# Optimization experiments

Measured on AMD Instinct MI355X. Metric: run time of the kernel, lower is better.

Reference implementation:

```python
import jax, jax.numpy as jnp
import numpy as np

N, E, Nd, D, F = 100000, 400000, 4096, 512, 8000
EMB = 300
NUM_LAYERS = 5


def setup_inputs() -> dict:
    key = jax.random.key(0)
    ks = iter(jax.random.split(key, 24))
    x = jax.random.randint(next(ks), (N, 2), 0, 3)
    edge_index = jax.random.randint(next(ks), (2, E), 0, N)
    edge_attr = jax.random.randint(next(ks), (E, 2), 0, 3)
    dangling_idx = jax.random.randint(next(ks), (Nd,), 0, N)
    frag_batch = jnp.sort(jax.random.randint(next(ks), (N,), 0, F))
    dangling_edge_index = jax.random.randint(next(ks), (2, D), 0, Nd)
    drop_edge_attr = jax.random.randint(next(ks), (D, 2), 0, 3)
    p = lambda shape: jax.random.normal(next(ks), shape, jnp.float32) * 0.02
    return dict(
        x=x, edge_index=edge_index, edge_attr=edge_attr,
        dangling_idx=dangling_idx, frag_batch=frag_batch,
        dangling_edge_index=dangling_edge_index, drop_edge_attr=drop_edge_attr,
        atom_emb1=p((120, EMB)), atom_emb2=p((3, EMB)),
        gin_ee1=p((NUM_LAYERS, 6, EMB)), gin_ee2=p((NUM_LAYERS, 3, EMB)),
        W1=p((NUM_LAYERS, EMB, 2 * EMB)), b1=jnp.zeros((NUM_LAYERS, 2 * EMB), jnp.float32),
        W2=p((NUM_LAYERS, 2 * EMB, EMB)), b2=jnp.zeros((NUM_LAYERS, EMB), jnp.float32),
        bn_g=jnp.ones((NUM_LAYERS, EMB), jnp.float32), bn_b=jnp.zeros((NUM_LAYERS, EMB), jnp.float32),
        E1=p((6, 4 * EMB * EMB)), E2=p((3, 4 * EMB * EMB)),
    )


def _gnn(x, edge_index, edge_attr, atom_emb1, atom_emb2,
         gin_ee1, gin_ee2, W1, b1, W2, b2, bn_g, bn_b):
    # node features from two categorical embeddings
    h = atom_emb1[x[:, 0]] + atom_emb2[x[:, 1]]  # [N, EMB]
    src, dst = edge_index[0], edge_index[1]
    for l in range(NUM_LAYERS):
        ee = gin_ee1[l][edge_attr[:, 0]] + gin_ee2[l][edge_attr[:, 1]]  # [E, EMB]
        aggr = jax.ops.segment_sum(h[src] + ee, dst, num_segments=N)
        # self-loops with edge_attr = (4, 0)
        aggr = aggr + h + gin_ee1[l][4] + gin_ee2[l][0]
        h = jax.nn.relu(aggr @ W1[l] + b1[l]) @ W2[l] + b2[l]  # GIN MLP
        # BatchNorm1d (training-mode batch statistics), eps=1e-5
        mean = h.mean(axis=0)
        var = h.var(axis=0)
        h = (h - mean) * jax.lax.rsqrt(var + 1e-5) * bn_g[l] + bn_b[l]
        if l < NUM_LAYERS - 1:
            h = jax.nn.relu(h)
    return h


def reference(x, edge_index, edge_attr, dangling_idx, frag_batch,
              dangling_edge_index, drop_edge_attr,
              atom_emb1, atom_emb2, gin_ee1, gin_ee2,
              W1, b1, W2, b2, bn_g, bn_b, E1, E2):
    h = _gnn(x, edge_index, edge_attr, atom_emb1, atom_emb2,
             gin_ee1, gin_ee2, W1, b1, W2, b2, bn_g, bn_b)  # [N, EMB]
    dangling_out = h[dangling_idx]  # [Nd, EMB]
    # global_mean_pool over fragments
    seg_sum = jax.ops.segment_sum(h, frag_batch, num_segments=F)
    cnt = jax.ops.segment_sum(jnp.ones((N, 1), h.dtype), frag_batch, num_segments=F)
    frag_mean = seg_sum / jnp.maximum(cnt, 1.0)
    frag_out = frag_mean[frag_batch][dangling_idx]  # [Nd, EMB]
    out = jnp.concatenate([dangling_out, frag_out], axis=1) / EMB  # [Nd, 2*EMB]
    out0 = out[dangling_edge_index[0]]  # [D, 2*EMB]
    # per-edge dynamic weight matrices [D, 2*EMB, 2*EMB]
    pm = (E1[drop_edge_attr[:, 0]] + E2[drop_edge_attr[:, 1]]).reshape(D, 2 * EMB, 2 * EMB)
    out0 = jnp.einsum('dk,dkm->dm', out0, pm)
    out1 = out[dangling_edge_index[1]]
    out2 = jnp.roll(out1, 1, axis=0)  # shift_k fixed to 1 for determinism
    logits = jnp.concatenate([jnp.sum(out0 * out1, axis=1),
                              jnp.sum(out0 * out2, axis=1)], axis=0)  # [2*D]
    return logits
```

## Files before the change

### kernel.cpp

```cpp
#include <hip/hip_runtime.h>
#include <hip/hip_bf16.h>
#include <stdint.h>

#define NN 100000
#define EE 400000
#define ND 4096
#define DD 512
#define FF 8000
#define EMB 300
#define HID 600
#define NL 5
#define TCH 50176
#define MPAD 100096

typedef unsigned short u16;
typedef _Float16 f16x8 __attribute__((ext_vector_type(8)));
typedef float f32x4 __attribute__((ext_vector_type(4)));
typedef float f32x2 __attribute__((ext_vector_type(2)));

static __device__ inline u16 f2h(float v) {
    union { _Float16 h; u16 u; } c; c.h = (_Float16)v; return c.u;
}
static __device__ inline float h2f(u16 u) {
    union { u16 u; _Float16 h; } c; c.u = u; return (float)c.h;
}
static __device__ inline uint32_t pk2(float a, float b) {
    return (uint32_t)f2h(a) | ((uint32_t)f2h(b) << 16);
}
static __device__ inline f32x2 up2(uint32_t w) {
    f32x2 r; r.x = h2f((u16)(w & 0xffff)); r.y = h2f((u16)(w >> 16)); return r;
}
static __device__ inline int loff(int row, int cb) {
    return row * 32 + ((cb ^ ((row >> 1) & 3)) * 8);
}

static __global__ void k_init_h(const int* __restrict__ x, const float* __restrict__ ae1,
                                const float* __restrict__ ae2, uint32_t* __restrict__ h) {
    int idx = blockIdx.x * 256 + threadIdx.x;
    if (idx >= NN * 160) return;
    int n = idx / 160, cw = idx - n * 160;
    int c = 2 * cw;
    int x0 = x[2 * n], x1 = x[2 * n + 1];
    float v0 = 0.f, v1 = 0.f;
    if (c < EMB)     v0 = ae1[x0 * EMB + c] + ae2[x1 * EMB + c];
    if (c + 1 < EMB) v1 = ae1[x0 * EMB + c + 1] + ae2[x1 * EMB + c + 1];
    h[idx] = pk2(v0, v1);
}

static __global__ void k_count(const int* __restrict__ ei, const int* __restrict__ ea,
                               int* __restrict__ deg, int* __restrict__ cnt1, int* __restrict__ cnt2) {
    int e = blockIdx.x * 256 + threadIdx.x;
    if (e >= EE) return;
    int dst = ei[EE + e];
    atomicAdd(&deg[dst], 1);
    atomicAdd(&cnt1[dst * 3 + ea[2 * e]], 1);
    atomicAdd(&cnt2[dst * 3 + ea[2 * e + 1]], 1);
}

static __global__ void k_scan1(const int* __restrict__ in, int* __restrict__ incl,
                               int* __restrict__ bsum, int L) {
    __shared__ int s[256];
    int t = threadIdx.x, i = blockIdx.x * 256 + t;
    int v = (i < L) ? in[i] : 0;
    s[t] = v; __syncthreads();
    for (int o = 1; o < 256; o <<= 1) {
        int xv = (t >= o) ? s[t - o] : 0; __syncthreads();
        s[t] += xv; __syncthreads();
    }
    if (i < L) incl[i] = s[t];
    if (t == 255) bsum[blockIdx.x] = s[255];
}

static __global__ void k_scan2(const int* __restrict__ bsum, int* __restrict__ boff, int nb) {
    __shared__ int s[1024];
    int t = threadIdx.x;
    int v = (t < nb) ? bsum[t] : 0;
    s[t] = v; __syncthreads();
    for (int o = 1; o < 1024; o <<= 1) {
        int xv = (t >= o) ? s[t - o] : 0; __syncthreads();
        s[t] += xv; __syncthreads();
    }
    if (t < nb) boff[t] = s[t] - v;
}

static __global__ void k_scan3(const int* __restrict__ in, const int* __restrict__ incl,
                               const int* __restrict__ boff, int* __restrict__ op,
                               int* __restrict__ cursor, int L) {
    int i = blockIdx.x * 256 + threadIdx.x;
    if (i >= L) return;
    int ex = incl[i] - in[i] + boff[i / 256];
    op[i] = ex;
    if (cursor) cursor[i] = ex;
    if (i == L - 1) op[L] = ex + in[i];
}

static __global__ void k_scatter(const int* __restrict__ ei, int* __restrict__ cursor,
                                 int* __restrict__ col) {
    int e = blockIdx.x * 256 + threadIdx.x;
    if (e >= EE) return;
    int dst = ei[EE + e], src = ei[e];
    int p = atomicAdd(&cursor[dst], 1);
    col[p] = src;
}

static __global__ void k_aggr(const u16* __restrict__ h, u16* __restrict__ ag,
                              const int* __restrict__ rowptr, const int* __restrict__ col,
                              const int* __restrict__ cnt1, const int* __restrict__ cnt2,
                              const float* __restrict__ ge1l, const float* __restrict__ ge2l,
                              const float* __restrict__ scv, int relu) {
    __shared__ float se[7 * 320];
    for (int idx = threadIdx.x; idx < 7 * 320; idx += 256) {
        int g = idx / 320, c = idx - g * 320;
        float v = 0.f;
        if (c < EMB) {
            if (g < 3) v = ge1l[g * EMB + c];
            else if (g < 6) v = ge2l[(g - 3) * EMB + c];
            else v = ge1l[4 * EMB + c] + ge2l[c];
        }
        se[idx] = v;
    }
    __syncthreads();
    int wv = threadIdx.x >> 6, lane = threadIdx.x & 63;

    int cw[3];
    f32x2 sc2[3], sh2[3];
#pragma unroll
    for (int j = 0; j < 3; j++) {
        cw[j] = lane + 64 * j;
        if (cw[j] < 160) {
            int c = 2 * cw[j];
            if (scv) {
                sc2[j] = *(const f32x2*)&scv[c];
                sh2[j] = *(const f32x2*)&scv[320 + c];
            } else { sc2[j] = (f32x2){1.f, 1.f}; sh2[j] = (f32x2){0.f, 0.f}; }
        }
    }

    for (int g0 = blockIdx.x * 4; g0 < NN; g0 += gridDim.x * 4) {
        int n = g0 + wv;
        if (n >= NN) continue;
        float c1a = (float)cnt1[n * 3], c1b = (float)cnt1[n * 3 + 1], c1c = (float)cnt1[n * 3 + 2];
        float c2a = (float)cnt2[n * 3], c2b = (float)cnt2[n * 3 + 1], c2c = (float)cnt2[n * 3 + 2];

        f32x2 acc[3];
        const uint32_t* hn = (const uint32_t*)(h + (size_t)n * 320);
#pragma unroll
        for (int j = 0; j < 3; j++) {
            if (cw[j] < 160) {
                int c = 2 * cw[j];
                f32x2 v = up2(hn[cw[j]]) * sc2[j] + sh2[j];
                if (relu) { v.x = fmaxf(v.x, 0.f); v.y = fmaxf(v.y, 0.f); }
                acc[j] = v + *(const f32x2*)&se[6 * 320 + c]
                       + c1a * *(const f32x2*)&se[c]
                       + c1b * *(const f32x2*)&se[320 + c]
                       + c1c * *(const f32x2*)&se[640 + c]
                       + c2a * *(const f32x2*)&se[960 + c]
                       + c2b * *(const f32x2*)&se[1280 + c]
                       + c2c * *(const f32x2*)&se[1600 + c];
            }
        }
        int p = rowptr[n], end = rowptr[n + 1];
        for (; p + 4 <= end; p += 4) {
            const uint32_t* h0 = (const uint32_t*)(h + (size_t)col[p] * 320);
            const uint32_t* h1 = (const uint32_t*)(h + (size_t)col[p + 1] * 320);
            const uint32_t* h2 = (const uint32_t*)(h + (size_t)col[p + 2] * 320);
            const uint32_t* h3 = (const uint32_t*)(h + (size_t)col[p + 3] * 320);
            uint32_t w0[3], w1[3], w2[3], w3[3];
#pragma unroll
            for (int j = 0; j < 3; j++) {
                if (cw[j] < 160) {
                    w0[j] = h0[cw[j]]; w1[j] = h1[cw[j]];
                    w2[j] = h2[cw[j]]; w3[j] = h3[cw[j]];
                }
            }
#pragma unroll
            for (int j = 0; j < 3; j++) {
                if (cw[j] < 160) {
                    f32x2 v0 = up2(w0[j]) * sc2[j] + sh2[j];
                    if (relu) { v0.x = fmaxf(v0.x, 0.f); v0.y = fmaxf(v0.y, 0.f); }
                    acc[j] += v0;
                    f32x2 v1 = up2(w1[j]) * sc2[j] + sh2[j];
                    if (relu) { v1.x = fmaxf(v1.x, 0.f); v1.y = fmaxf(v1.y, 0.f); }
                    acc[j] += v1;
                    f32x2 v2 = up2(w2[j]) * sc2[j] + sh2[j];
                    if (relu) { v2.x = fmaxf(v2.x, 0.f); v2.y = fmaxf(v2.y, 0.f); }
                    acc[j] += v2;
                    f32x2 v3 = up2(w3[j]) * sc2[j] + sh2[j];
                    if (relu) { v3.x = fmaxf(v3.x, 0.f); v3.y = fmaxf(v3.y, 0.f); }
                    acc[j] += v3;
                }
            }
        }
        for (; p + 2 <= end; p += 2) {
            const uint32_t* h0 = (const uint32_t*)(h + (size_t)col[p] * 320);
            const uint32_t* h1 = (const uint32_t*)(h + (size_t)col[p + 1] * 320);
            uint32_t w0[3], w1[3];
#pragma unroll
            for (int j = 0; j < 3; j++)
                if (cw[j] < 160) { w0[j] = h0[cw[j]]; w1[j] = h1[cw[j]]; }
#pragma unroll
            for (int j = 0; j < 3; j++) {
                if (cw[j] < 160) {
                    f32x2 v0 = up2(w0[j]) * sc2[j] + sh2[j];
                    if (relu) { v0.x = fmaxf(v0.x, 0.f); v0.y = fmaxf(v0.y, 0.f); }
                    acc[j] += v0;
                    f32x2 v1 = up2(w1[j]) * sc2[j] + sh2[j];
                    if (relu) { v1.x = fmaxf(v1.x, 0.f); v1.y = fmaxf(v1.y, 0.f); }
                    acc[j] += v1;
                }
            }
        }
        for (; p < end; ++p) {
            const uint32_t* hr = (const uint32_t*)(h + (size_t)col[p] * 320);
#pragma unroll
            for (int j = 0; j < 3; j++) {
                if (cw[j] < 160) {
                    f32x2 v = up2(hr[cw[j]]) * sc2[j] + sh2[j];
                    if (relu) { v.x = fmaxf(v.x, 0.f); v.y = fmaxf(v.y, 0.f); }
                    acc[j] += v;
                }
            }
        }
        uint32_t* ao = (uint32_t*)(ag + (size_t)n * 320);
#pragma unroll
        for (int j = 0; j < 3; j++)
            if (cw[j] < 160) ao[cw[j]] = pk2(acc[j].x, acc[j].y);
    }
}

static __global__ void k_packW1(const float* __restrict__ W1, u16* __restrict__ W1p) {
    int idx = blockIdx.x * 256 + threadIdx.x;
    const int per = 640 * 320;
    if (idx >= NL * per) return;
    int l = idx / per, rem = idx % per;
    int n = rem / 320, k = rem % 320;
    float v = (k < EMB && n < HID) ? W1[(size_t)l * EMB * HID + (size_t)k * HID + n] : 0.f;
    W1p[idx] = f2h(v);
}

static __global__ void k_packW2(const float* __restrict__ W2, u16* __restrict__ W2p) {
    int idx = blockIdx.x * 256 + threadIdx.x;
    const int per = 384 * 640;
    if (idx >= NL * per) return;
    int l = idx / per, rem = idx % per;
    int n = rem / 640, k = rem % 640;
    float v = (k < HID && n < EMB) ? W2[(size_t)l * HID * EMB + (size_t)k * EMB + n] : 0.f;
    W2p[idx] = f2h(v);
}

static __global__ void k_packb(const float* __restrict__ b1, const float* __restrict__ b2,
                               float* __restrict__ b1p, float* __restrict__ b2p) {
    int idx = blockIdx.x * 256 + threadIdx.x;
    if (idx < NL * 640) {
        int l = idx / 640, n = idx % 640;
        b1p[idx] = (n < HID) ? b1[l * HID + n] : 0.f;
    } else if (idx < NL * 640 + NL * 384) {
        int j = idx - NL * 640;
        int l = j / 384, n = j % 384;
        b2p[j] = (n < EMB) ? b2[l * EMB + n] : 0.f;
    }
}

static __global__ void k_precompMt(const float* __restrict__ E1, const float* __restrict__ E2,
                                   u16* __restrict__ Mpt) {
    __shared__ float sT[32][33];
    int p = blockIdx.x, mt = blockIdx.y, kt = blockIdx.z;
    int a = p / 3, b = p % 3;
    const float* e1 = E1 + (size_t)a * 360000;
    const float* e2 = E2 + (size_t)b * 360000;
    int tx = threadIdx.x & 31, ty = threadIdx.x >> 5;
#pragma unroll
    for (int it = 0; it < 4; it++) {
        int k = kt * 32 + ty + it * 8;
        int m = mt * 32 + tx;
        float v = 0.f;
        if (k < HID && m < HID) v = e1[k * HID + m] + e2[k * HID + m];
        sT[ty + it * 8][tx] = v;
    }
    __syncthreads();
#pragma unroll
    for (int it = 0; it < 4; it++) {
        int m = mt * 32 + ty + it * 8;
        int k = kt * 32 + tx;
        Mpt[(size_t)p * 640 * 640 + (size_t)m * 640 + k] = f2h(sT[tx][ty + it * 8]);
    }
}

template <int MODE>
static __global__ __launch_bounds__(256) void k_mfma(
        const u16* __restrict__ A, const u16* __restrict__ B,
        const float* __restrict__ bias, u16* __restrict__ Out, int Mc,
        float* __restrict__ colsum, float* __restrict__ colsq) {
    constexpr int BM    = (MODE == 1) ? 128 : 64;
    constexpr int STR   = (MODE == 1) ? 320 : 640;
    constexpr int STRO  = (MODE == 1) ? 640 : 320;
    constexpr int NSTEP = (MODE == 1) ? 10 : 20;
    constexpr int MF = 4;
    constexpr int NF = (MODE == 1) ? 4 : 2;

    __shared__ __align__(16) u16 sA[BM * 32];
    __shared__ __align__(16) u16 sB[128 * 32];

    int tid = threadIdx.x;
    int lane = tid & 63, wv = tid >> 6;
    int wm = (MODE == 1) ? (wv >> 1) : 0;
    int wn = (MODE == 1) ? (wv & 1) : wv;
    int m0 = blockIdx.y * BM;
    int n0 = blockIdx.x * 128;
    int sr = tid >> 2, scb = tid & 3;

    uint4 rA0, rA1, rB0, rB1;
    auto do_load = [&](int ks) {
        int kk = ks * 32;
        const u16* as = A + (size_t)(m0 + sr) * STR + kk + scb * 8;
        rA0 = *(const uint4*)as;
        if (MODE == 1) rA1 = *(const uint4*)(as + (size_t)64 * STR);
        const u16* bs = B + (size_t)(n0 + sr) * STR + kk + scb * 8;
        rB0 = *(const uint4*)bs;
        rB1 = *(const uint4*)(bs + (size_t)64 * STR);
    };
    do_load(0);

    f32x4 acc[MF][NF];
#pragma unroll
    for (int i = 0; i < MF; i++)
#pragma unroll
        for (int j = 0; j < NF; j++) {
            acc[i][j][0] = 0.f; acc[i][j][1] = 0.f; acc[i][j][2] = 0.f; acc[i][j][3] = 0.f;
        }

    int lrow = lane & 15, lcb = lane >> 4;
    for (int ks = 0; ks < NSTEP; ++ks) {
        __syncthreads();
        *(uint4*)&sA[loff(sr, scb)] = rA0;
        if (MODE == 1) *(uint4*)&sA[loff(sr + 64, scb)] = rA1;
        *(uint4*)&sB[loff(sr, scb)] = rB0;
        *(uint4*)&sB[loff(sr + 64, scb)] = rB1;
        __syncthreads();
        if (ks + 1 < NSTEP) do_load(ks + 1);
        f16x8 af[MF], bfr[NF];
#pragma unroll
        for (int mf = 0; mf < MF; ++mf) {
            int r = wm * 64 + mf * 16 + lrow;
            af[mf] = *(const f16x8*)&sA[loff(r, lcb)];
        }
#pragma unroll
        for (int nf = 0; nf < NF; ++nf) {
            int r = wn * (NF * 16) + nf * 16 + lrow;
            bfr[nf] = *(const f16x8*)&sB[loff(r, lcb)];
        }
#pragma unroll
        for (int mf = 0; mf < MF; ++mf)
#pragma unroll
            for (int nf = 0; nf < NF; ++nf)
                acc[mf][nf] = __builtin_amdgcn_mfma_f32_16x16x32_f16(af[mf], bfr[nf], acc[mf][nf], 0, 0, 0);
    }

    int lrow4 = (lane >> 4) * 4, lcol = lane & 15;
    if (MODE == 1) {
#pragma unroll
        for (int mf = 0; mf < MF; ++mf)
#pragma unroll
            for (int nf = 0; nf < NF; ++nf) {
                int colg = n0 + wn * 64 + nf * 16 + lcol;
                float bv = bias[colg];
#pragma unroll
                for (int rg = 0; rg < 4; ++rg) {
                    int rowl = m0 + wm * 64 + mf * 16 + lrow4 + rg;
                    float v = fmaxf(acc[mf][nf][rg] + bv, 0.f);
                    Out[(size_t)rowl * STRO + colg] = f2h(v);
                }
            }
    } else {
#pragma unroll
        for (int nf = 0; nf < NF; ++nf) {
            int colg = n0 + wn * 32 + nf * 16 + lcol;
            float bv = bias[colg];
            float s = 0.f, q = 0.f;
#pragma unroll
            for (int mf = 0; mf < MF; ++mf)
#pragma unroll
                for (int rg = 0; rg < 4; ++rg) {
                    int rowl = m0 + mf * 16 + lrow4 + rg;
                    float v = acc[mf][nf][rg] + bv;
                    if (rowl < Mc) {
                        s += v; q += v * v;
                        if (colg < EMB) Out[(size_t)rowl * STRO + colg] = f2h(v);
                    }
                }
            s += __shfl_xor(s, 16); s += __shfl_xor(s, 32);
            q += __shfl_xor(q, 16); q += __shfl_xor(q, 32);
            if (lane < 16) { atomicAdd(&colsum[colg], s); atomicAdd(&colsq[colg], q); }
        }
    }
}

static __global__ void k_bnfinal(const float* __restrict__ colsum, const float* __restrict__ colsq,
                                 const float* __restrict__ g, const float* __restrict__ b,
                                 float* __restrict__ scv) {
    int c = threadIdx.x;
    if (c >= 320) return;
    if (c >= EMB) { scv[c] = 0.f; scv[320 + c] = 0.f; return; }
    float mean = colsum[c] * (1.f / NN);
    float var = colsq[c] * (1.f / NN) - mean * mean;
    float rs = rsqrtf(var + 1e-5f);
    float sc = rs * g[c];
    scv[c] = sc;
    scv[320 + c] = b[c] - mean * sc;
}

static __global__ void k_fragcnt(const int* __restrict__ fb, int* __restrict__ fcnt) {
    int i = blockIdx.x * 256 + threadIdx.x;
    if (i >= NN) return;
    atomicAdd(&fcnt[fb[i]], 1);
}

static __global__ void k_fragmean(const u16* __restrict__ h, const int* __restrict__ fstart,
                                  const float* __restrict__ scv, float* __restrict__ fm) {
    int wv = threadIdx.x >> 6, lane = threadIdx.x & 63;
    int f = blockIdx.x * 4 + wv;
    if (f >= FF) return;
    int beg = fstart[f], end = fstart[f + 1];
    float inv = (end > beg) ? 1.f / (float)(end - beg) : 0.f;
    float a0[3], a1[3]; int cw[3];
#pragma unroll
    for (int j = 0; j < 3; j++) { cw[j] = lane + 64 * j; a0[j] = 0.f; a1[j] = 0.f; }
    for (int r = beg; r < end; ++r) {
        const uint32_t* hr = (const uint32_t*)(h + (size_t)r * 320);
#pragma unroll
        for (int j = 0; j < 3; j++)
            if (cw[j] < 160) {
                uint32_t hv = hr[cw[j]];
                a0[j] += h2f((u16)(hv & 0xffff)); a1[j] += h2f((u16)(hv >> 16));
            }
    }
#pragma unroll
    for (int j = 0; j < 3; j++) {
        int c = 2 * cw[j];
        if (c < EMB)
            fm[(size_t)f * EMB + c] = (end > beg) ? (a0[j] * inv * scv[c] + scv[320 + c]) : 0.f;
        if (c + 1 < EMB)
            fm[(size_t)f * EMB + c + 1] = (end > beg) ? (a1[j] * inv * scv[c + 1] + scv[321 + c]) : 0.f;
    }
}

static __global__ void k_build_out(const u16* __restrict__ h, const float* __restrict__ fm,
                                   const int* __restrict__ didx, const int* __restrict__ fb,
                                   const float* __restrict__ scv, u16* __restrict__ outb16) {
    int idx = blockIdx.x * 256 + threadIdx.x;
    if (idx >= ND * 640) return;
    int d = idx / 640, c = idx - d * 640;
    int n = didx[d];
    float v = 0.f;
    if (c < EMB)          v = (h2f(h[(size_t)n * 320 + c]) * scv[c] + scv[320 + c]) * (1.f / EMB);
    else if (c < 2 * EMB) v = fm[(size_t)fb[n] * EMB + (c - EMB)] * (1.f / EMB);
    outb16[idx] = f2h(v);
}

static __global__ void k_bucket(const int* __restrict__ dea, int* __restrict__ eord,
                                int* __restrict__ tm, int* __restrict__ ntl) {
    __shared__ int cnt[9], off[9], cur[9];
    __shared__ short pe[DD];
    int tid = threadIdx.x;
    for (int i = tid; i < 768; i += 256) eord[i] = -1;
    if (tid < 9) { cnt[tid] = 0; cur[tid] = 0; }
    __syncthreads();
    for (int e = tid; e < DD; e += 256) {
        int p = dea[2 * e] * 3 + dea[2 * e + 1];
        pe[e] = (short)p;
        atomicAdd(&cnt[p], 1);
    }
    __syncthreads();
    if (tid == 0) {
        int o = 0, tt = 0;
        for (int p = 0; p < 9; p++) {
            off[p] = o;
            int nt = (cnt[p] + 15) >> 4;
            for (int t = 0; t < nt; t++) { tm[2 * tt] = p; tm[2 * tt + 1] = o + 16 * t; tt++; }
            o += nt * 16;
        }
        *ntl = tt;
    }
    __syncthreads();
    for (int e = tid; e < DD; e += 256) {
        int p = pe[e];
        int slot = off[p] + atomicAdd(&cur[p], 1);
        eord[slot] = e;
    }
}

static __global__ void k_vgather(const u16* __restrict__ outb16, const int* __restrict__ eord,
                                 const int* __restrict__ dei, u16* __restrict__ Vg) {
    int idx = blockIdx.x * 256 + threadIdx.x;
    if (idx >= 768 * 80) return;
    int slot = idx / 80, cb = idx - slot * 80;
    int d = eord[slot];
    uint4 v = {0u, 0u, 0u, 0u};
    if (d >= 0) v = *(const uint4*)&outb16[(size_t)dei[d] * 640 + cb * 8];
    *(uint4*)&Vg[(size_t)slot * 640 + cb * 8] = v;
}

static __global__ __launch_bounds__(256) void k_out0m(
        const u16* __restrict__ Vg, const u16* __restrict__ Mpt,
        const int* __restrict__ tm, const int* __restrict__ ntl,
        const int* __restrict__ eord, float* __restrict__ o0) {
    int bx = blockIdx.x;
    if (bx >= *ntl) return;
    int p = tm[2 * bx], row0 = tm[2 * bx + 1];
    __shared__ __align__(16) u16 sA[16 * 32];
    __shared__ __align__(16) u16 sB[640 * 32];
    int tid = threadIdx.x, lane = tid & 63, wv = tid >> 6;
    const u16* Bb = Mpt + (size_t)p * 640 * 640;
    f32x4 acc[10];
#pragma unroll
    for (int j = 0; j < 10; j++) { acc[j][0]=0.f; acc[j][1]=0.f; acc[j][2]=0.f; acc[j][3]=0.f; }
    int lrow = lane & 15, lcb = lane >> 4;
    for (int ks = 0; ks < 20; ks++) {
        int kk = ks * 32;
        __syncthreads();
        if (tid < 64) {
            int row = tid >> 2, cb = tid & 3;
            *(uint4*)&sA[loff(row, cb)] = *(const uint4*)&Vg[(size_t)(row0 + row) * 640 + kk + cb * 8];
        }
#pragma unroll
        for (int j = 0; j < 10; j++) {
            int i = tid + j * 256, row = i >> 2, cb = i & 3;
            *(uint4*)&sB[loff(row, cb)] = *(const uint4*)&Bb[(size_t)row * 640 + kk + cb * 8];
        }
        __syncthreads();
        f16x8 af = *(const f16x8*)&sA[loff(lrow, lcb)];
#pragma unroll
        for (int nf = 0; nf < 10; nf++) {
            f16x8 bf = *(const f16x8*)&sB[loff(wv * 160 + nf * 16 + lrow, lcb)];
            acc[nf] = __builtin_amdgcn_mfma_f32_16x16x32_f16(af, bf, acc[nf], 0, 0, 0);
        }
    }
    int lrow4 = (lane >> 4) * 4, lcol = lane & 15;
#pragma unroll
    for (int nf = 0; nf < 10; nf++) {
        int col = wv * 160 + nf * 16 + lcol;
#pragma unroll
        for (int rg = 0; rg < 4; rg++) {
            int row = lrow4 + rg;
            int e = eord[row0 + row];
            if (e >= 0 && col < HID) o0[(size_t)e * 640 + col] = acc[nf][rg];
        }
    }
}

static __global__ void k_logits(const float* __restrict__ o0, const u16* __restrict__ outb16,
                                const int* __restrict__ dei, float* __restrict__ dout) {
    int d = blockIdx.x;
    int tid = threadIdx.x, lane = tid & 63;
    int which = tid >> 6;
    int dsel = which ? (d + DD - 1) % DD : d;
    const float* a = o0 + (size_t)d * 640;
    const u16* bv = outb16 + (size_t)dei[DD + dsel] * 640;
    float s = 0.f;
    for (int c = lane; c < HID; c += 64) s += a[c] * h2f(bv[c]);
    for (int o = 32; o > 0; o >>= 1) s += __shfl_down(s, o);
    if (lane == 0) dout[which ? DD + d : d] = s;
}

extern "C" void kernel_launch(void* const* d_in, const int* in_sizes, int n_in,
                              void* d_out, int out_size, void* d_ws, size_t ws_size,
                              hipStream_t stream) {
    const int* x    = (const int*)d_in[0];
    const int* ei   = (const int*)d_in[1];
    const int* ea   = (const int*)d_in[2];
    const int* didx = (const int*)d_in[3];
    const int* fb   = (const int*)d_in[4];
    const int* dei  = (const int*)d_in[5];
    const int* dea  = (const int*)d_in[6];
    const float* ae1 = (const float*)d_in[7];
    const float* ae2 = (const float*)d_in[8];
    const float* ge1 = (const float*)d_in[9];
    const float* ge2 = (const float*)d_in[10];
    const float* W1  = (const float*)d_in[11];
    const float* b1  = (const float*)d_in[12];
    const float* W2  = (const float*)d_in[13];
    const float* b2  = (const float*)d_in[14];
    const float* bng = (const float*)d_in[15];
    const float* bnb = (const float*)d_in[16];
    const float* E1  = (const float*)d_in[17];
    const float* E2  = (const float*)d_in[18];
    float* dout = (float*)d_out;

    char* w = (char*)d_ws;
    auto alloc = [&](size_t bytes) -> void* {
        void* p = (void*)w;
        w += (bytes + 255) & ~(size_t)255;
        return p;
    };
    u16* h   = (u16*)alloc((size_t)MPAD * 320 * 2);
    u16* ag  = (u16*)alloc((size_t)MPAD * 320 * 2);
    u16* t   = (u16*)alloc((size_t)TCH * 640 * 2);
    u16* W1p = (u16*)alloc((size_t)NL * 640 * 320 * 2);
    u16* W2p = (u16*)alloc((size_t)NL * 384 * 640 * 2);
    u16* Mpt = (u16*)alloc((size_t)9 * 640 * 640 * 2);
    float* b1p = (float*)alloc((size_t)NL * 640 * 4);
    float* b2p = (float*)alloc((size_t)NL * 384 * 4);
    int* rowptr = (int*)alloc((size_t)(NN + 1) * 4);
    int* cursor = (int*)alloc((size_t)NN * 4);
    int* col    = (int*)alloc((size_t)EE * 4);
    int* deg    = (int*)alloc((size_t)NN * 4);
    int* cnt1   = (int*)alloc((size_t)NN * 3 * 4);
    int* cnt2   = (int*)alloc((size_t)NN * 3 * 4);
    int* incl   = (int*)alloc((size_t)NN * 4);
    int* bsum   = (int*)alloc(4096);
    int* boff   = (int*)alloc(4096);
    int* fcnt   = (int*)alloc((size_t)FF * 4);
    int* fstart = (int*)alloc((size_t)(FF + 1) * 4);
    float* colsum = (float*)alloc(384 * 4);
    float* colsq  = (float*)alloc(384 * 4);
    float* scv    = (float*)alloc(640 * 4);
    int* eord = (int*)alloc(768 * 4);
    int* tm   = (int*)alloc(96 * 4);
    int* ntl  = (int*)alloc(256);
    char* ov = (char*)t;
    auto oalloc = [&](size_t bytes) -> void* {
        void* p = (void*)ov;
        ov += (bytes + 255) & ~(size_t)255;
        return p;
    };
    float* fragmean = (float*)oalloc((size_t)FF * EMB * 4);
    u16* outb16     = (u16*)oalloc((size_t)ND * 640 * 2);
    float* o0       = (float*)oalloc((size_t)DD * 640 * 4);
    u16* Vg         = (u16*)oalloc((size_t)768 * 640 * 2);

    hipMemsetAsync(deg, 0, (size_t)NN * 4, stream);
    hipMemsetAsync(cnt1, 0, (size_t)NN * 3 * 4, stream);
    hipMemsetAsync(cnt2, 0, (size_t)NN * 3 * 4, stream);
    hipMemsetAsync(fcnt, 0, (size_t)FF * 4, stream);

    k_packW1<<<(NL * 640 * 320 + 255) / 256, 256, 0, stream>>>(W1, W1p);
    k_packW2<<<(NL * 384 * 640 + 255) / 256, 256, 0, stream>>>(W2, W2p);
    k_packb<<<(NL * (640 + 384) + 255) / 256, 256, 0, stream>>>(b1, b2, b1p, b2p);
    k_precompMt<<<dim3(9, 20, 20), 256, 0, stream>>>(E1, E2, Mpt);
    k_bucket<<<1, 256, 0, stream>>>(dea, eord, tm, ntl);

    k_init_h<<<(NN * 160 + 255) / 256, 256, 0, stream>>>(x, ae1, ae2, (uint32_t*)h);
    k_count<<<(EE + 255) / 256, 256, 0, stream>>>(ei, ea, deg, cnt1, cnt2);

    int nb = (NN + 255) / 256;
    k_scan1<<<nb, 256, 0, stream>>>(deg, incl, bsum, NN);
    k_scan2<<<1, 1024, 0, stream>>>(bsum, boff, nb);
    k_scan3<<<nb, 256, 0, stream>>>(deg, incl, boff, rowptr, cursor, NN);
    k_scatter<<<(EE + 255) / 256, 256, 0, stream>>>(ei, cursor, col);

    k_fragcnt<<<nb, 256, 0, stream>>>(fb, fcnt);
    int nbf = (FF + 255) / 256;
    k_scan1<<<nbf, 256, 0, stream>>>(fcnt, incl, bsum, FF);
    k_scan2<<<1, 1024, 0, stream>>>(bsum, boff, nbf);
    k_scan3<<<nbf, 256, 0, stream>>>(fcnt, incl, boff, fstart, (int*)nullptr, FF);

    for (int l = 0; l < NL; l++) {
        const float* ge1l = ge1 + (size_t)l * 6 * EMB;
        const float* ge2l = ge2 + (size_t)l * 3 * EMB;
        k_aggr<<<2048, 256, 0, stream>>>(h, ag, rowptr, col, cnt1, cnt2, ge1l, ge2l,
                                         (l == 0) ? nullptr : scv, (l == 0) ? 0 : 1);
        hipMemsetAsync(colsum, 0, 384 * 4, stream);
        hipMemsetAsync(colsq, 0, 384 * 4, stream);
        for (int c0 = 0; c0 < NN; c0 += TCH) {
            int Mc = (NN - c0 < TCH) ? (NN - c0) : TCH;
            int mt1 = (Mc + 127) / 128;
            k_mfma<1><<<dim3(5, mt1), 256, 0, stream>>>(
                ag + (size_t)c0 * 320, W1p + (size_t)l * 640 * 320, b1p + l * 640,
                t, Mc, nullptr, nullptr);
            int mt2 = (Mc + 63) / 64;
            k_mfma<2><<<dim3(3, mt2), 256, 0, stream>>>(
                t, W2p + (size_t)l * 384 * 640, b2p + l * 384,
                h + (size_t)c0 * 320, Mc, colsum, colsq);
        }
        k_bnfinal<<<1, 320, 0, stream>>>(colsum, colsq, bng + (size_t)l * EMB, bnb + (size_t)l * EMB, scv);
    }

    k_fragmean<<<(FF + 3) / 4, 256, 0, stream>>>(h, fstart, scv, fragmean);
    k_build_out<<<(ND * 640 + 255) / 256, 256, 0, stream>>>(h, fragmean, didx, fb, scv, outb16);
    k_vgather<<<(768 * 80 + 255) / 256, 256, 0, stream>>>(outb16, eord, dei, Vg);
    k_out0m<<<48, 256, 0, stream>>>(Vg, Mpt, tm, ntl, eord, o0);
    k_logits<<<DD, 128, 0, stream>>>(o0, outb16, dei, dout);
}
```

Before: 1.766 ms.

## Fuse GIN MLP's two GEMMs into one kernel keeping hidden tile in LDS

Replaces the two chunked MFMA GEMM launches per layer with one fused kernel. Each 512-thread block computes a 64-row tile of relu(A·W1+b1) into a swizzled 80KB LDS buffer, then multiplies it by W2 and accumulates the BatchNorm column statistics. This removes the global round trip of the 600-wide hidden activation and the chunk loop. In exchange, each block reloads all of W1 and W2 per 64 rows, and the large LDS footprint limits occupancy to about one block per CU.

```diff
diff --git a/kernel.cpp b/kernel.cpp
--- a/kernel.cpp
+++ b/kernel.cpp
@@ -10,7 +10,6 @@
 #define EMB 300
 #define HID 600
 #define NL 5
-#define TCH 50176
 #define MPAD 100096
 
 typedef unsigned short u16;
@@ -286,112 +285,135 @@
     }
 }
 
-template <int MODE>
-static __global__ __launch_bounds__(256) void k_mfma(
-        const u16* __restrict__ A, const u16* __restrict__ B,
-        const float* __restrict__ bias, u16* __restrict__ Out, int Mc,
-        float* __restrict__ colsum, float* __restrict__ colsq) {
-    constexpr int BM    = (MODE == 1) ? 128 : 64;
-    constexpr int STR   = (MODE == 1) ? 320 : 640;
-    constexpr int STRO  = (MODE == 1) ? 640 : 320;
-    constexpr int NSTEP = (MODE == 1) ? 10 : 20;
-    constexpr int MF = 4;
-    constexpr int NF = (MODE == 1) ? 4 : 2;
-
-    __shared__ __align__(16) u16 sA[BM * 32];
-    __shared__ __align__(16) u16 sB[128 * 32];
-
-    int tid = threadIdx.x;
-    int lane = tid & 63, wv = tid >> 6;
-    int wm = (MODE == 1) ? (wv >> 1) : 0;
-    int wn = (MODE == 1) ? (wv & 1) : wv;
-    int m0 = blockIdx.y * BM;
-    int n0 = blockIdx.x * 128;
-    int sr = tid >> 2, scb = tid & 3;
-
-    uint4 rA0, rA1, rB0, rB1;
-    auto do_load = [&](int ks) {
+static __global__ __launch_bounds__(512) void k_mlp(
+        const u16* __restrict__ A, const u16* __restrict__ W1pl, const float* __restrict__ b1l,
+        const u16* __restrict__ W2pl, const float* __restrict__ b2l,
+        u16* __restrict__ H, float* __restrict__ colsum, float* __restrict__ colsq) {
+    __shared__ __align__(16) u16 sA[64 * 32];
+    __shared__ __align__(16) u16 sB[640 * 32];
+    __shared__ __align__(16) u16 tl[64 * 640];
+    int tid = threadIdx.x, lane = tid & 63, w = tid >> 6;
+    int m0 = blockIdx.x * 64;
+    int lrow = lane & 15, lcb = lane >> 4;
+    int lrow4 = (lane >> 4) * 4, lcol = lane & 15;
+
+    uint4 rA, rB[5];
+    auto load1 = [&](int ks) {
         int kk = ks * 32;
-        const u16* as = A + (size_t)(m0 + sr) * STR + kk + scb * 8;
-        rA0 = *(const uint4*)as;
-        if (MODE == 1) rA1 = *(const uint4*)(as + (size_t)64 * STR);
-        const u16* bs = B + (size_t)(n0 + sr) * STR + kk + scb * 8;
-        rB0 = *(const uint4*)bs;
-        rB1 = *(const uint4*)(bs + (size_t)64 * STR);
+        if (tid < 256) {
+            int row = tid >> 2, cb = tid & 3;
+            rA = *(const uint4*)&A[(size_t)(m0 + row) * 320 + kk + cb * 8];
+        }
+#pragma unroll
+        for (int j = 0; j < 5; j++) {
+            int idx = tid + 512 * j, row = idx >> 2, cb = idx & 3;
+            rB[j] = *(const uint4*)&W1pl[(size_t)row * 320 + kk + cb * 8];
+        }
     };
-    do_load(0);
-
-    f32x4 acc[MF][NF];
-#pragma unroll
-    for (int i = 0; i < MF; i++)
-#pragma unroll
-        for (int j = 0; j < NF; j++) {
-            acc[i][j][0] = 0.f; acc[i][j][1] = 0.f; acc[i][j][2] = 0.f; acc[i][j][3] = 0.f;
-        }
-
-    int lrow = lane & 15, lcb = lane >> 4;
-    for (int ks = 0; ks < NSTEP; ++ks) {
+    load1(0);
+    f32x4 acc[4][5];
+#pragma unroll
+    for (int i = 0; i < 4; i++)
+#pragma unroll
+        for (int j = 0; j < 5; j++) { acc[i][j][0]=0.f; acc[i][j][1]=0.f; acc[i][j][2]=0.f; acc[i][j][3]=0.f; }
+
+    for (int ks = 0; ks < 10; ++ks) {
         __syncthreads();
-        *(uint4*)&sA[loff(sr, scb)] = rA0;
-        if (MODE == 1) *(uint4*)&sA[loff(sr + 64, scb)] = rA1;
-        *(uint4*)&sB[loff(sr, scb)] = rB0;
-        *(uint4*)&sB[loff(sr + 64, scb)] = rB1;
+        if (tid < 256) { int row = tid >> 2, cb = tid & 3; *(uint4*)&sA[loff(row, cb)] = rA; }
+#pragma unroll
+        for (int j = 0; j < 5; j++) {
+            int idx = tid + 512 * j, row = idx >> 2, cb = idx & 3;
+            *(uint4*)&sB[loff(row, cb)] = rB[j];
+        }
         __syncthreads();
-        if (ks + 1 < NSTEP) do_load(ks + 1);
-        f16x8 af[MF], bfr[NF];
-#pragma unroll
-        for (int mf = 0; mf < MF; ++mf) {
-            int r = wm * 64 + mf * 16 + lrow;
-            af[mf] = *(const f16x8*)&sA[loff(r, lcb)];
-        }
-#pragma unroll
-        for (int nf = 0; nf < NF; ++nf) {
-            int r = wn * (NF * 16) + nf * 16 + lrow;
-            bfr[nf] = *(const f16x8*)&sB[loff(r, lcb)];
-        }
-#pragma unroll
-        for (int mf = 0; mf < MF; ++mf)
-#pragma unroll
-            for (int nf = 0; nf < NF; ++nf)
-                acc[mf][nf] = __builtin_amdgcn_mfma_f32_16x16x32_f16(af[mf], bfr[nf], acc[mf][nf], 0, 0, 0);
-    }
-
-    int lrow4 = (lane >> 4) * 4, lcol = lane & 15;
-    if (MODE == 1) {
-#pragma unroll
-        for (int mf = 0; mf < MF; ++mf)
-#pragma unroll
-            for (int nf = 0; nf < NF; ++nf) {
-                int colg = n0 + wn * 64 + nf * 16 + lcol;
-                float bv = bias[colg];
-#pragma unroll
-                for (int rg = 0; rg < 4; ++rg) {
-                    int rowl = m0 + wm * 64 + mf * 16 + lrow4 + rg;
-                    float v = fmaxf(acc[mf][nf][rg] + bv, 0.f);
-                    Out[(size_t)rowl * STRO + colg] = f2h(v);
+        if (ks + 1 < 10) load1(ks + 1);
+        f16x8 af[4], bf[5];
+#pragma unroll
+        for (int mf = 0; mf < 4; mf++) af[mf] = *(const f16x8*)&sA[loff(mf * 16 + lrow, lcb)];
+#pragma unroll
+        for (int nf = 0; nf < 5; nf++) bf[nf] = *(const f16x8*)&sB[loff(w * 80 + nf * 16 + lrow, lcb)];
+#pragma unroll
+        for (int mf = 0; mf < 4; mf++)
+#pragma unroll
+            for (int nf = 0; nf < 5; nf++)
+                acc[mf][nf] = __builtin_amdgcn_mfma_f32_16x16x32_f16(af[mf], bf[nf], acc[mf][nf], 0, 0, 0);
+    }
+#pragma unroll
+    for (int nf = 0; nf < 5; nf++) {
+        int col = w * 80 + nf * 16 + lcol;
+        float bv = b1l[col];
+        int blk = col >> 3, elem = col & 7;
+#pragma unroll
+        for (int mf = 0; mf < 4; mf++)
+#pragma unroll
+            for (int rg = 0; rg < 4; rg++) {
+                int row = mf * 16 + lrow4 + rg;
+                float v = fmaxf(acc[mf][nf][rg] + bv, 0.f);
+                tl[(row * 80 + (blk ^ (row & 7))) * 8 + elem] = f2h(v);
+            }
+    }
+
+    uint4 rB2[3];
+    auto load2 = [&](int ks) {
+        int kk = ks * 32;
+#pragma unroll
+        for (int j = 0; j < 3; j++) {
+            int idx = tid + 512 * j, row = idx >> 2, cb = idx & 3;
+            rB2[j] = *(const uint4*)&W2pl[(size_t)row * 640 + kk + cb * 8];
+        }
+    };
+    load2(0);
+    f32x4 acc2[2][5];
+#pragma unroll
+    for (int i = 0; i < 2; i++)
+#pragma unroll
+        for (int j = 0; j < 5; j++) { acc2[i][j][0]=0.f; acc2[i][j][1]=0.f; acc2[i][j][2]=0.f; acc2[i][j][3]=0.f; }
+    int wm2 = w >> 2, wn2 = w & 3;
+
+    for (int ks = 0; ks < 20; ++ks) {
+        __syncthreads();
+#pragma unroll
+        for (int j = 0; j < 3; j++) {
+            int idx = tid + 512 * j, row = idx >> 2, cb = idx & 3;
+            *(uint4*)&sB[loff(row, cb)] = rB2[j];
+        }
+        __syncthreads();
+        if (ks + 1 < 20) load2(ks + 1);
+        f16x8 af2[2], bf2[5];
+#pragma unroll
+        for (int mf = 0; mf < 2; mf++) {
+            int r = wm2 * 32 + mf * 16 + lrow;
+            int unit = r * 80 + ((ks * 4 + lcb) ^ (r & 7));
+            af2[mf] = *(const f16x8*)&tl[unit * 8];
+        }
+#pragma unroll
+        for (int nf = 0; nf < 5; nf++) bf2[nf] = *(const f16x8*)&sB[loff(wn2 * 80 + nf * 16 + lrow, lcb)];
+#pragma unroll
+        for (int mf = 0; mf < 2; mf++)
+#pragma unroll
+            for (int nf = 0; nf < 5; nf++)
+                acc2[mf][nf] = __builtin_amdgcn_mfma_f32_16x16x32_f16(af2[mf], bf2[nf], acc2[mf][nf], 0, 0, 0);
+    }
+
+#pragma unroll
+    for (int nf = 0; nf < 5; nf++) {
+        int colg = wn2 * 80 + nf * 16 + lcol;
+        float bv = b2l[colg];
+        float s = 0.f, q = 0.f;
+#pragma unroll
+        for (int mf = 0; mf < 2; mf++)
+#pragma unroll
+            for (int rg = 0; rg < 4; rg++) {
+                int rowg = m0 + wm2 * 32 + mf * 16 + lrow4 + rg;
+                float v = acc2[mf][nf][rg] + bv;
+                if (rowg < NN) {
+                    s += v; q += v * v;
+                    if (colg < EMB) H[(size_t)rowg * 320 + colg] = f2h(v);
                 }
             }
-    } else {
-#pragma unroll
-        for (int nf = 0; nf < NF; ++nf) {
-            int colg = n0 + wn * 32 + nf * 16 + lcol;
-            float bv = bias[colg];
-            float s = 0.f, q = 0.f;
-#pragma unroll
-            for (int mf = 0; mf < MF; ++mf)
-#pragma unroll
-                for (int rg = 0; rg < 4; ++rg) {
-                    int rowl = m0 + mf * 16 + lrow4 + rg;
-                    float v = acc[mf][nf][rg] + bv;
-                    if (rowl < Mc) {
-                        s += v; q += v * v;
-                        if (colg < EMB) Out[(size_t)rowl * STRO + colg] = f2h(v);
-                    }
-                }
-            s += __shfl_xor(s, 16); s += __shfl_xor(s, 32);
-            q += __shfl_xor(q, 16); q += __shfl_xor(q, 32);
-            if (lane < 16) { atomicAdd(&colsum[colg], s); atomicAdd(&colsq[colg], q); }
-        }
+        s += __shfl_xor(s, 16); s += __shfl_xor(s, 32);
+        q += __shfl_xor(q, 16); q += __shfl_xor(q, 32);
+        if (lane < 16) { atomicAdd(&colsum[colg], s); atomicAdd(&colsq[colg], q); }
     }
 }
 
@@ -594,7 +616,7 @@
     };
     u16* h   = (u16*)alloc((size_t)MPAD * 320 * 2);
     u16* ag  = (u16*)alloc((size_t)MPAD * 320 * 2);
-    u16* t   = (u16*)alloc((size_t)TCH * 640 * 2);
+    char* tail = (char*)alloc((size_t)20 * 1024 * 1024);
     u16* W1p = (u16*)alloc((size_t)NL * 640 * 320 * 2);
     u16* W2p = (u16*)alloc((size_t)NL * 384 * 640 * 2);
     u16* Mpt = (u16*)alloc((size_t)9 * 640 * 640 * 2);
@@ -617,7 +639,7 @@
     int* eord = (int*)alloc(768 * 4);
     int* tm   = (int*)alloc(96 * 4);
     int* ntl  = (int*)alloc(256);
-    char* ov = (char*)t;
+    char* ov = tail;
     auto oalloc = [&](size_t bytes) -> void* {
         void* p = (void*)ov;
         ov += (bytes + 255) & ~(size_t)255;
@@ -654,6 +676,7 @@
     k_scan2<<<1, 1024, 0, stream>>>(bsum, boff, nbf);
     k_scan3<<<nbf, 256, 0, stream>>>(fcnt, incl, boff, fstart, (int*)nullptr, FF);
 
+    const int MT = (NN + 63) / 64;
     for (int l = 0; l < NL; l++) {
         const float* ge1l = ge1 + (size_t)l * 6 * EMB;
         const float* ge2l = ge2 + (size_t)l * 3 * EMB;
@@ -661,17 +684,9 @@
                                          (l == 0) ? nullptr : scv, (l == 0) ? 0 : 1);
         hipMemsetAsync(colsum, 0, 384 * 4, stream);
         hipMemsetAsync(colsq, 0, 384 * 4, stream);
-        for (int c0 = 0; c0 < NN; c0 += TCH) {
-            int Mc = (NN - c0 < TCH) ? (NN - c0) : TCH;
-            int mt1 = (Mc + 127) / 128;
-            k_mfma<1><<<dim3(5, mt1), 256, 0, stream>>>(
-                ag + (size_t)c0 * 320, W1p + (size_t)l * 640 * 320, b1p + l * 640,
-                t, Mc, nullptr, nullptr);
-            int mt2 = (Mc + 63) / 64;
-            k_mfma<2><<<dim3(3, mt2), 256, 0, stream>>>(
-                t, W2p + (size_t)l * 384 * 640, b2p + l * 384,
-                h + (size_t)c0 * 320, Mc, colsum, colsq);
-        }
+        k_mlp<<<MT, 512, 0, stream>>>(ag, W1p + (size_t)l * 640 * 320, b1p + l * 640,
+                                      W2p + (size_t)l * 384 * 640, b2p + l * 384,
+                                      h, colsum, colsq);
         k_bnfinal<<<1, 320, 0, stream>>>(colsum, colsq, bng + (size_t)l * EMB, bnb + (size_t)l * EMB, scv);
     }
 
```

Result: slower. 2.781 ms (+57.5%).
